# Performance work log

Measured on AMD Instinct MI355X. Metric: run time of the kernel, lower is better.

The kernel has to match this reference:

```python
import jax, jax.numpy as jnp
import numpy as np

LOG_SIG_MIN, LOG_SIG_MAX = -20.0, 2.0
BN_EPS = 1e-5

def leaky_relu(x):
    return jnp.where(x >= 0, x, 0.01 * x)

def setup_inputs() -> dict:
    key = jax.random.key(0)
    ks = jax.random.split(key, 12)
    E, B, N, H, A = 8, 16384, 64, 512, 8  # encoders, batch, nagents, hidden, heads
    d = H // A
    f32 = jnp.float32
    inp = {}
    inp['states'] = jax.random.normal(ks[0], (E, B, N), dtype=f32)
    inp['pre_actions'] = jax.random.normal(ks[1], (B, H), dtype=f32)
    inp['W_enc'] = jax.random.normal(ks[2], (E, N, H), dtype=f32) / np.sqrt(N)
    inp['b_enc'] = jnp.zeros((E, H), dtype=f32)
    inp['W_pre'] = jax.random.normal(ks[3], (H, H), dtype=f32) / np.sqrt(H)
    inp['b_pre'] = jnp.zeros((H,), dtype=f32)
    inp['Wk'] = jax.random.normal(ks[4], (A, H, d), dtype=f32) / np.sqrt(H)
    inp['Wsel'] = jax.random.normal(ks[5], (A, H, d), dtype=f32) / np.sqrt(H)
    inp['Wv'] = jax.random.normal(ks[6], (A, H, d), dtype=f32) / np.sqrt(H)
    inp['bv'] = jnp.zeros((A, d), dtype=f32)
    inp['W_actor'] = jax.random.normal(ks[7], (H, H), dtype=f32) / np.sqrt(H)
    inp['b_actor'] = jnp.zeros((H,), dtype=f32)
    inp['W_mean'] = jax.random.normal(ks[8], (H, N), dtype=f32) / np.sqrt(H)
    inp['b_mean'] = jnp.zeros((N,), dtype=f32)
    inp['W_logstd'] = jax.random.normal(ks[9], (H, N), dtype=f32) / np.sqrt(H)
    inp['b_logstd'] = jnp.zeros((N,), dtype=f32)
    return inp

def reference(states, pre_actions, W_enc, b_enc, W_pre, b_pre, Wk, Wsel, Wv, bv,
              W_actor, b_actor, W_mean, b_mean, W_logstd, b_logstd):
    # states: [E, B, N]; per-encoder BatchNorm1d (training-mode batch stats, no affine)
    mu = states.mean(axis=1, keepdims=True)                      # [E,1,N]
    var = states.var(axis=1, keepdims=True)                      # biased var, as torch BN
    s_norm = (states - mu) * jax.lax.rsqrt(var + BN_EPS)
    # per-encoder Linear + LeakyReLU -> encodings [E, B, H]
    encs = leaky_relu(jnp.einsum('ebn,enh->ebh', s_norm, W_enc) + b_enc[:, None, :])
    # per-head keys/values over all encoders: [A, E, B, d]
    keys = jnp.einsum('ebh,ahd->aebd', encs, Wk)
    vals = leaky_relu(jnp.einsum('ebh,ahd->aebd', encs, Wv) + bv[:, None, None, :])
    # selector from encoded previous actions: [A, B, d]
    pre = leaky_relu(pre_actions @ W_pre + b_pre)                 # [B, H]
    sel = jnp.einsum('bh,ahd->abd', pre, Wsel)
    d = keys.shape[-1]
    logits = jnp.einsum('abd,aebd->abe', sel, keys)               # [A, B, E]
    w = jax.nn.softmax(logits / np.sqrt(d), axis=-1)
    attn = jnp.einsum('aebd,abe->abd', vals, w)                   # [A, B, d]
    B = attn.shape[1]
    actor_in = jnp.transpose(attn, (1, 0, 2)).reshape(B, -1)      # [B, A*d] head-concat
    x = jax.nn.relu(actor_in @ W_actor + b_actor)
    mean = x @ W_mean + b_mean
    log_std = jnp.clip(x @ W_logstd + b_logstd, LOG_SIG_MIN, LOG_SIG_MAX)
    return mean, log_std, actor_in
```

## Files before the change

### kernel.cpp

```cpp
#include <hip/hip_runtime.h>
#include <hip/hip_bf16.h>
#include <stdint.h>

#define E_ 8
#define B_ 16384
#define N_ 64
#define H_ 512
#define A_ 8
#define D_ 64

typedef __hip_bfloat16 bf16;
typedef __attribute__((ext_vector_type(8))) short s8v;
typedef __attribute__((ext_vector_type(4))) float f4v;

__device__ __forceinline__ float bf2f(bf16 v) { return __bfloat162float(v); }
__device__ __forceinline__ bf16 f2bf(float v) { return __float2bfloat16(v); }
__device__ __forceinline__ short f2bfs(float v) {
    bf16 b = f2bf(v); short s; __builtin_memcpy(&s, &b, 2); return s;
}
__device__ __forceinline__ float bfs2f(short s) {
    bf16 b; __builtin_memcpy(&b, &s, 2); return bf2f(b);
}

__device__ __forceinline__ void async_load16(const void* g, void* l) {
    __builtin_amdgcn_global_load_lds(
        (const __attribute__((address_space(1))) void*)g,
        (__attribute__((address_space(3))) void*)l, 16, 0, 0);
}

__device__ __forceinline__ int swz_off(int row, int krow) {
    return row * 64 + (((krow >> 3) ^ (row & 7)) << 3);
}

__device__ __forceinline__ int swz32(int row, int g) {
    return row * 32 + ((g ^ ((row >> 1) & 3)) << 3);
}

template <int CB>
__device__ __forceinline__ void xcd_map(int x, int nBm, int& bm, int& bn) {
    if ((nBm & 7) == 0) {
        int j = x & 7, s = x >> 3;
        bn = s & ((1 << CB) - 1);
        bm = ((s >> CB) << 3) | j;
    } else {
        bm = x >> CB;
        bn = x & ((1 << CB) - 1);
    }
}

__global__ __launch_bounds__(256) void bnPart(const float* __restrict__ states,
                                              float* __restrict__ part,
                                              bf16* __restrict__ sbf) {
    int blk = blockIdx.x;
    int e = blk >> 6, sl = blk & 63;
    int tid = threadIdx.x, n = tid & 63, rg = tid >> 6;
    const long rowBase = (long)e * B_ + (long)sl * 256;
    const float* base = states + rowBase * 64;
    float s1 = 0.f, s2 = 0.f;
    for (int i = 0; i < 64; ++i) {
        float v = base[(rg + i * 4) * 64 + n];
        s1 += v; s2 += v * v;
        sbf[(rowBase + rg + i * 4) * 64 + n] = f2bf(v);
    }
    __shared__ float sh[2][4][64];
    sh[0][rg][n] = s1; sh[1][rg][n] = s2;
    __syncthreads();
    if (tid < 64) {
        float t1 = sh[0][0][n] + sh[0][1][n] + sh[0][2][n] + sh[0][3][n];
        float t2 = sh[1][0][n] + sh[1][1][n] + sh[1][2][n] + sh[1][3][n];
        part[((long)blk * 64 + n) * 2 + 0] = t1;
        part[((long)blk * 64 + n) * 2 + 1] = t2;
    }
}

__global__ void bnFin(const float* __restrict__ part, float* __restrict__ mu_rstd) {
    int idx = blockIdx.x * blockDim.x + threadIdx.x;
    if (idx >= E_ * 64) return;
    int e = idx >> 6, n = idx & 63;
    float s1 = 0.f, s2 = 0.f;
    for (int sl = 0; sl < 64; ++sl) {
        s1 += part[(((long)e * 64 + sl) * 64 + n) * 2 + 0];
        s2 += part[(((long)e * 64 + sl) * 64 + n) * 2 + 1];
    }
    float mu = s1 / (float)B_;
    float var = s2 / (float)B_ - mu * mu;
    mu_rstd[idx * 2 + 0] = mu;
    mu_rstd[idx * 2 + 1] = rsqrtf(var + 1e-5f);
}

__global__ void foldEnc(const float* __restrict__ W_enc, const float* __restrict__ b_enc,
                        const float* __restrict__ mu_rstd,
                        bf16* __restrict__ WencfT, float* __restrict__ bencf) {
    int idx = blockIdx.x * 256 + threadIdx.x;
    int e = idx >> 9, h = idx & 511;
    float acc = b_enc[e * 512 + h];
    for (int n = 0; n < 64; ++n) {
        float mu = mu_rstd[(e * 64 + n) * 2 + 0];
        float rs = mu_rstd[(e * 64 + n) * 2 + 1];
        float w = W_enc[((long)e * 64 + n) * 512 + h];
        WencfT[((long)e * 512 + h) * 64 + n] = f2bf(w * rs);
        acc -= mu * rs * w;
    }
    bencf[e * 512 + h] = acc;
}

__global__ __launch_bounds__(256) void packAll(
    const float* __restrict__ W_pre, const float* __restrict__ W_actor,
    const float* __restrict__ Wsel, const float* __restrict__ Wk,
    const float* __restrict__ Wv, const float* __restrict__ wm,
    const float* __restrict__ wl, const float* __restrict__ pre_actions,
    bf16* __restrict__ WpreT, bf16* __restrict__ WactorT, bf16* __restrict__ WselT,
    bf16* __restrict__ WkvaT, bf16* __restrict__ WmlT, bf16* __restrict__ pa_bf) {
    int bx = blockIdx.x, tid = threadIdx.x;
    if (bx < 2048) {
        const float* in = (bx < 1024) ? W_pre : W_actor;
        bf16* out = (bx < 1024) ? WpreT : WactorT;
        int idx = (bx & 1023) * 256 + tid;
        int n = idx >> 9, k = idx & 511;
        out[idx] = f2bf(in[k * 512 + n]);
    } else if (bx < 3072) {
        int idx = (bx - 2048) * 256 + tid;
        int n = idx >> 9, h = idx & 511;
        int a = n >> 6, dd = n & 63;
        WselT[idx] = f2bf(Wsel[((long)a * 512 + h) * 64 + dd]);
    } else if (bx < 5120) {
        int idx = (bx - 3072) * 256 + tid;
        int n = idx >> 9, h = idx & 511;
        int a = n >> 7, j = n & 127;
        const float* src = (j < 64) ? Wk : Wv;
        WkvaT[idx] = f2bf(src[((long)a * 512 + h) * 64 + (j & 63)]);
    } else if (bx < 5376) {
        int idx = (bx - 5120) * 256 + tid;
        int n = idx >> 9, k = idx & 511;
        float v = (n < 64) ? wm[k * 64 + n] : wl[k * 64 + (n - 64)];
        WmlT[idx] = f2bf(v);
    } else {
        int i = (bx - 5376) * 256 + tid;
        float4 v = ((const float4*)pre_actions)[i];
        bf16 o[4] = {f2bf(v.x), f2bf(v.y), f2bf(v.z), f2bf(v.w)};
        __builtin_memcpy(pa_bf + (long)i * 4, o, 8);
    }
}

template <int ACT, int OUTF, bool HAS_BIAS, int CB>
__global__ __launch_bounds__(256) void gemm_bt(
    const bf16* __restrict__ Ag, const bf16* __restrict__ Bg,
    const float* __restrict__ bias, const float* __restrict__ bias2,
    void* __restrict__ out, void* __restrict__ out2,
    int M, int Nn, int K, long sA, long sB, long sBias, long sO) {
    const int tid = threadIdx.x, lane = tid & 63, wid = tid >> 6;
    const int wm = wid >> 1, wn = wid & 1;
    int bm, bn;
    xcd_map<CB>(blockIdx.x, gridDim.x >> CB, bm, bn);
    const int bz = blockIdx.z;
    const bf16* Aptr = Ag + (long)bz * sA + (long)bm * 128 * K;
    const bf16* Bptr = Bg + (long)bz * sB + (long)bn * 128 * K;

    __shared__ __align__(16) short sAl[128 * 64];
    __shared__ __align__(16) short sBl[128 * 64];

    const int srow = lane >> 3;
    const int scol = (((lane & 7) ^ srow) << 3);

    f4v acc[4][4];
#pragma unroll
    for (int i = 0; i < 4; ++i)
#pragma unroll
        for (int j = 0; j < 4; ++j) acc[i][j] = f4v{0.f, 0.f, 0.f, 0.f};

    for (int k0 = 0; k0 < K; k0 += 64) {
#pragma unroll
        for (int i = 0; i < 4; ++i) {
            int r = (wid * 4 + i) * 8 + srow;
            async_load16(Aptr + (long)r * K + k0 + scol, (char*)sAl + (wid * 4 + i) * 1024);
            async_load16(Bptr + (long)r * K + k0 + scol, (char*)sBl + (wid * 4 + i) * 1024);
        }
        __syncthreads();
#pragma unroll
        for (int kk = 0; kk < 64; kk += 32) {
            int krow = kk + (lane >> 4) * 8;
            s8v af[4], bfr[4];
#pragma unroll
            for (int mi = 0; mi < 4; ++mi)
                af[mi] = *(const s8v*)(sAl + swz_off(wm * 64 + mi * 16 + (lane & 15), krow));
#pragma unroll
            for (int ni = 0; ni < 4; ++ni)
                bfr[ni] = *(const s8v*)(sBl + swz_off(wn * 64 + ni * 16 + (lane & 15), krow));
#pragma unroll
            for (int mi = 0; mi < 4; ++mi)
#pragma unroll
                for (int ni = 0; ni < 4; ++ni)
                    acc[mi][ni] = __builtin_amdgcn_mfma_f32_16x16x32_bf16(
                        af[mi], bfr[ni], acc[mi][ni], 0, 0, 0);
        }
        __syncthreads();
    }

    long m0 = (long)bm * 128 + wm * 64;
    long n0 = (long)bn * 128 + wn * 64;
#pragma unroll
    for (int mi = 0; mi < 4; ++mi)
#pragma unroll
        for (int ni = 0; ni < 4; ++ni)
#pragma unroll
            for (int r = 0; r < 4; ++r) {
                long gm = m0 + mi * 16 + (lane >> 4) * 4 + r;
                long gn = n0 + ni * 16 + (lane & 15);
                float v = acc[mi][ni][r];
                if constexpr (HAS_BIAS) v += bias[sBias * bz + gn];
                if constexpr (ACT == 1) v = (v >= 0.f) ? v : 0.01f * v;
                if constexpr (ACT == 2) v = fmaxf(v, 0.f);
                if constexpr (OUTF == 0) {
                    ((bf16*)out)[(long)bz * sO + gm * Nn + gn] = f2bf(v);
                } else if constexpr (OUTF == 1) {
                    ((float*)out)[(long)bz * sO + gm * Nn + gn] = v;
                } else if constexpr (OUTF == 2) {
                    if (gn < 64) {
                        ((float*)out)[gm * 64 + gn] = v + bias[gn];
                    } else {
                        float w = v + bias2[gn - 64];
                        w = fminf(fmaxf(w, -20.f), 2.f);
                        ((float*)out2)[gm * 64 + (gn - 64)] = w;
                    }
                } else {
                    ((bf16*)out)[(gm * E_ + bz) * 512 + gn] = f2bf(v);
                }
            }
}

__global__ __launch_bounds__(256, 4) void kv_attn(
    const bf16* __restrict__ Ag, const bf16* __restrict__ Bg,
    const float* __restrict__ bv, const float* __restrict__ sel,
    float* __restrict__ actor_f32, bf16* __restrict__ attn_bf, int b0) {
    const int tid = threadIdx.x, lane = tid & 63, wid = tid >> 6;
    const int wm = wid >> 1, wn = wid & 1;
    int bm, a;
    xcd_map<3>(blockIdx.x, gridDim.x >> 3, bm, a);
    const bf16* Aptr = Ag + (long)bm * 128 * 512;
    const bf16* Bptr = Bg + (long)a * 128 * 512;

    __shared__ __align__(16) short smem[17408];
    __shared__ float lgs[128];

    const long bgBase = (long)b0 + (long)bm * 16;

    auto stage = [&](int kt, int buf) {
#pragma unroll
        for (int i = 0; i < 2; ++i) {
            int c = tid + i * 256;
            int r = c >> 2;
            int g = (c & 3) ^ ((r >> 1) & 3);
            async_load16(Aptr + (long)r * 512 + kt * 32 + g * 8,
                         (char*)smem + buf * 8192 + c * 16);
            async_load16(Bptr + (long)r * 512 + kt * 32 + g * 8,
                         (char*)smem + 16384 + buf * 8192 + c * 16);
        }
    };

    f4v acc[4][4];
#pragma unroll
    for (int i = 0; i < 4; ++i)
#pragma unroll
        for (int j = 0; j < 4; ++j) acc[i][j] = f4v{0.f, 0.f, 0.f, 0.f};

    stage(0, 0);
    __syncthreads();
    int cur = 0;
    for (int t = 0; t < 16; ++t) {
        if (t < 15) stage(t + 1, cur ^ 1);
        const short* sAc = smem + cur * 4096;
        const short* sBc = smem + 8192 + cur * 4096;
        const int g = lane >> 4;
        s8v af[4], bfr[4];
#pragma unroll
        for (int mi = 0; mi < 4; ++mi)
            af[mi] = *(const s8v*)(sAc + swz32(wm * 64 + mi * 16 + (lane & 15), g));
#pragma unroll
        for (int ni = 0; ni < 4; ++ni)
            bfr[ni] = *(const s8v*)(sBc + swz32(wn * 64 + ni * 16 + (lane & 15), g));
#pragma unroll
        for (int mi = 0; mi < 4; ++mi)
#pragma unroll
            for (int ni = 0; ni < 4; ++ni)
                acc[mi][ni] = __builtin_amdgcn_mfma_f32_16x16x32_bf16(
                    af[mi], bfr[ni], acc[mi][ni], 0, 0, 0);
        __syncthreads();
        cur ^= 1;
    }

    short* keysC = smem;
    short* vT    = smem + 9216;
    const int quad = lane >> 4, cl = lane & 15;
#pragma unroll
    for (int mi = 0; mi < 4; ++mi)
#pragma unroll
        for (int ni = 0; ni < 4; ++ni)
#pragma unroll
            for (int r = 0; r < 4; ++r) {
                int row = wm * 64 + mi * 16 + quad * 4 + r;
                float v = acc[mi][ni][r];
                if (wn == 0) {
                    keysC[row * 72 + ni * 16 + cl] = f2bfs(v);
                } else {
                    int d = ni * 16 + cl;
                    v += bv[a * 64 + d];
                    v = (v >= 0.f) ? v : 0.01f * v;
                    vT[d * 128 + (row ^ ((d & 15) << 3))] = f2bfs(v);
                }
            }

    s8v bselH[2], bselL[2];
#pragma unroll
    for (int kk = 0; kk < 2; ++kk) {
        const float* sp = sel + (bgBase + cl) * 512 + a * 64 + kk * 32 + quad * 8;
#pragma unroll
        for (int j = 0; j < 8; ++j) {
            float s = sp[j] * 0.125f;
            short h = f2bfs(s);
            bselH[kk][j] = h;
            bselL[kk][j] = f2bfs(s - bfs2f(h));
        }
    }
    __syncthreads();

    {
        f4v lgacc[2] = {f4v{0.f, 0.f, 0.f, 0.f}, f4v{0.f, 0.f, 0.f, 0.f}};
#pragma unroll
        for (int kk = 0; kk < 2; ++kk) {
#pragma unroll
            for (int mi = 0; mi < 2; ++mi) {
                s8v af = *(const s8v*)(keysC + (wid * 32 + mi * 16 + cl) * 72 +
                                       kk * 32 + quad * 8);
                lgacc[mi] = __builtin_amdgcn_mfma_f32_16x16x32_bf16(
                    af, bselH[kk], lgacc[mi], 0, 0, 0);
                lgacc[mi] = __builtin_amdgcn_mfma_f32_16x16x32_bf16(
                    af, bselL[kk], lgacc[mi], 0, 0, 0);
            }
        }
#pragma unroll
        for (int mi = 0; mi < 2; ++mi)
#pragma unroll
            for (int r = 0; r < 4; ++r) {
                int grow = wid * 32 + mi * 16 + quad * 4 + r;
                if (cl == (grow >> 3)) lgs[grow] = lgacc[mi][r];
            }
    }
    __syncthreads();

#pragma unroll
    for (int t = 0; t < 4; ++t) {
        int lb = wid * 4 + t, row0 = lb * 8;
        s8v vvv = *(const s8v*)(vT + lane * 128 + (row0 ^ ((lane & 15) << 3)));
        float lg[8], vv[8];
#pragma unroll
        for (int e = 0; e < 8; ++e) {
            vv[e] = bfs2f(vvv[e]);
            lg[e] = lgs[row0 + e];
        }
        float mx = lg[0];
#pragma unroll
        for (int e = 1; e < 8; ++e) mx = fmaxf(mx, lg[e]);
        float ssum = 0.f, w[8];
#pragma unroll
        for (int e = 0; e < 8; ++e) { w[e] = __expf(lg[e] - mx); ssum += w[e]; }
        float inv = 1.f / ssum;
        float at = 0.f;
#pragma unroll
        for (int e = 0; e < 8; ++e) at += vv[e] * (w[e] * inv);
        long o = (bgBase + lb) * 512 + a * 64 + lane;
        actor_f32[o] = at;
        attn_bf[o] = f2bf(at);
    }
}

extern "C" void kernel_launch(void* const* d_in, const int* in_sizes, int n_in,
                              void* d_out, int out_size, void* d_ws, size_t ws_size,
                              hipStream_t stream) {
    (void)in_sizes; (void)n_in; (void)out_size;
    const float* states      = (const float*)d_in[0];
    const float* pre_actions = (const float*)d_in[1];
    const float* W_enc       = (const float*)d_in[2];
    const float* b_enc       = (const float*)d_in[3];
    const float* W_pre       = (const float*)d_in[4];
    const float* b_pre       = (const float*)d_in[5];
    const float* Wk          = (const float*)d_in[6];
    const float* Wsel        = (const float*)d_in[7];
    const float* Wv          = (const float*)d_in[8];
    const float* bv          = (const float*)d_in[9];
    const float* W_actor     = (const float*)d_in[10];
    const float* b_actor     = (const float*)d_in[11];
    const float* W_mean      = (const float*)d_in[12];
    const float* b_mean      = (const float*)d_in[13];
    const float* W_logstd    = (const float*)d_in[14];
    const float* b_logstd    = (const float*)d_in[15];

    char* ws = (char*)d_ws;
    size_t off = 0;
    auto alloc = [&](size_t bytes) -> void* {
        void* p = ws + off;
        off = (off + bytes + 255) & ~(size_t)255;
        return p;
    };
    float* mu_rstd = (float*)alloc((size_t)E_ * 64 * 2 * 4);
    float* bnpart  = (float*)alloc((size_t)E_ * 64 * 64 * 2 * 4);
    bf16* WencfT   = (bf16*)alloc((size_t)E_ * 512 * 64 * 2);
    float* bencf   = (float*)alloc((size_t)E_ * 512 * 4);
    bf16* WpreT    = (bf16*)alloc((size_t)512 * 512 * 2);
    bf16* WselT    = (bf16*)alloc((size_t)512 * 512 * 2);
    bf16* WkvaT    = (bf16*)alloc((size_t)1024 * 512 * 2);
    bf16* WactorT  = (bf16*)alloc((size_t)512 * 512 * 2);
    bf16* WmlT     = (bf16*)alloc((size_t)128 * 512 * 2);
    bf16* pa_bf    = (bf16*)alloc((size_t)B_ * 512 * 2);
    bf16* p_pre    = (bf16*)alloc((size_t)B_ * 512 * 2);
    float* p_sel   = (float*)alloc((size_t)B_ * 512 * 4);
    bf16* s_bf     = (bf16*)alloc((size_t)E_ * B_ * 64 * 2);
    bf16* p_attn = pa_bf;
    bf16* p_x    = p_pre;

    size_t remaining = (ws_size > off) ? ws_size - off : 0;
    int Bc = B_;
    while (Bc > 128 && (size_t)Bc * 8192 + 4096 > remaining) Bc >>= 1;
    const int NC = B_ / Bc;
    bf16* c_encs = (bf16*)alloc((size_t)E_ * Bc * 512 * 2);

    packAll<<<13568, 256, 0, stream>>>(W_pre, W_actor, Wsel, Wk, Wv, W_mean, W_logstd,
                                       pre_actions, WpreT, WactorT, WselT, WkvaT, WmlT,
                                       pa_bf);
    bnPart<<<512, 256, 0, stream>>>(states, bnpart, s_bf);
    bnFin<<<2, 256, 0, stream>>>(bnpart, mu_rstd);
    foldEnc<<<16, 256, 0, stream>>>(W_enc, b_enc, mu_rstd, WencfT, bencf);

    gemm_bt<1, 0, true, 2><<<dim3((B_ / 128) << 2, 1, 1), 256, 0, stream>>>(
        pa_bf, WpreT, b_pre, nullptr, p_pre, nullptr, B_, 512, 512, 0, 0, 0, 0);
    gemm_bt<0, 1, false, 2><<<dim3((B_ / 128) << 2, 1, 1), 256, 0, stream>>>(
        p_pre, WselT, nullptr, nullptr, p_sel, nullptr, B_, 512, 512, 0, 0, 0, 0);

    float* actor_out = (float*)d_out + 2L * B_ * 64;
    for (int c = 0; c < NC; ++c) {
        int b0 = c * Bc;
        gemm_bt<1, 4, true, 2><<<dim3((Bc / 128) << 2, 1, E_), 256, 0, stream>>>(
            s_bf + (long)b0 * 64, WencfT, bencf, nullptr, c_encs, nullptr, Bc, 512, 64,
            (long)B_ * 64, (long)512 * 64, 512, 0);
        kv_attn<<<dim3((Bc / 16) * 8, 1, 1), 256, 0, stream>>>(
            c_encs, WkvaT, bv, p_sel, actor_out, p_attn, b0);
    }

    gemm_bt<2, 0, true, 2><<<dim3((B_ / 128) << 2, 1, 1), 256, 0, stream>>>(
        p_attn, WactorT, b_actor, nullptr, p_x, nullptr, B_, 512, 512, 0, 0, 0, 0);
    gemm_bt<0, 2, false, 0><<<dim3(B_ / 128, 1, 1), 256, 0, stream>>>(
        p_x, WmlT, b_mean, b_logstd, (float*)d_out, (float*)d_out + (long)B_ * 64,
        B_, 128, 512, 0, 0, 0, 0);
}
```

Measured before the change: 482.8 us.

## Double-buffer GEMM K-loop with 64x128 tiles and higher occupancy

Rewrites the shared GEMM kernel to use 64-row M tiles with K steps of 32, and double-buffers shared memory so the async global-to-LDS load of the next K tile overlaps the MFMA work on the current one. This removes one barrier per iteration and the load stall. Launch bounds now request 4 blocks per SM, and grids are doubled to match the smaller tiles. In exchange each tile reuses data less, so global traffic for the B operand rises, and register pressure is capped.

```diff
diff --git a/kernel.cpp b/kernel.cpp
--- a/kernel.cpp
+++ b/kernel.cpp
@@ -26,10 +26,6 @@
     __builtin_amdgcn_global_load_lds(
         (const __attribute__((address_space(1))) void*)g,
         (__attribute__((address_space(3))) void*)l, 16, 0, 0);
-}
-
-__device__ __forceinline__ int swz_off(int row, int krow) {
-    return row * 64 + (((krow >> 3) ^ (row & 7)) << 3);
 }
 
 __device__ __forceinline__ int swz32(int row, int g) {
@@ -143,7 +139,7 @@
 }
 
 template <int ACT, int OUTF, bool HAS_BIAS, int CB>
-__global__ __launch_bounds__(256) void gemm_bt(
+__global__ __launch_bounds__(256, 4) void gemm_bt2(
     const bf16* __restrict__ Ag, const bf16* __restrict__ Bg,
     const float* __restrict__ bias, const float* __restrict__ bias2,
     void* __restrict__ out, void* __restrict__ out2,
@@ -153,59 +149,70 @@
     int bm, bn;
     xcd_map<CB>(blockIdx.x, gridDim.x >> CB, bm, bn);
     const int bz = blockIdx.z;
-    const bf16* Aptr = Ag + (long)bz * sA + (long)bm * 128 * K;
+    const bf16* Aptr = Ag + (long)bz * sA + (long)bm * 64 * K;
     const bf16* Bptr = Bg + (long)bz * sB + (long)bn * 128 * K;
 
-    __shared__ __align__(16) short sAl[128 * 64];
-    __shared__ __align__(16) short sBl[128 * 64];
-
-    const int srow = lane >> 3;
-    const int scol = (((lane & 7) ^ srow) << 3);
-
-    f4v acc[4][4];
-#pragma unroll
-    for (int i = 0; i < 4; ++i)
+    __shared__ __align__(16) short smem[12288];
+
+    auto stage = [&](int kt, int buf) {
+        {
+            int c = tid, r = c >> 2;
+            int g = (c & 3) ^ ((r >> 1) & 3);
+            async_load16(Aptr + (long)r * K + kt * 32 + g * 8,
+                         (char*)smem + buf * 4096 + c * 16);
+        }
+#pragma unroll
+        for (int i = 0; i < 2; ++i) {
+            int c = tid + i * 256, r = c >> 2;
+            int g = (c & 3) ^ ((r >> 1) & 3);
+            async_load16(Bptr + (long)r * K + kt * 32 + g * 8,
+                         (char*)smem + 8192 + buf * 8192 + c * 16);
+        }
+    };
+
+    f4v acc[2][4];
+#pragma unroll
+    for (int i = 0; i < 2; ++i)
 #pragma unroll
         for (int j = 0; j < 4; ++j) acc[i][j] = f4v{0.f, 0.f, 0.f, 0.f};
 
-    for (int k0 = 0; k0 < K; k0 += 64) {
-#pragma unroll
-        for (int i = 0; i < 4; ++i) {
-            int r = (wid * 4 + i) * 8 + srow;
-            async_load16(Aptr + (long)r * K + k0 + scol, (char*)sAl + (wid * 4 + i) * 1024);
-            async_load16(Bptr + (long)r * K + k0 + scol, (char*)sBl + (wid * 4 + i) * 1024);
-        }
+    stage(0, 0);
+    __syncthreads();
+    int cur = 0;
+    const int nt = K >> 5;
+    for (int t = 0; t < nt; ++t) {
+        if (t < nt - 1) stage(t + 1, cur ^ 1);
+        const short* sAc = smem + cur * 2048;
+        const short* sBc = smem + 4096 + cur * 4096;
+        const int g = lane >> 4;
+        s8v af[2], bfr[4];
+#pragma unroll
+        for (int mi = 0; mi < 2; ++mi)
+            af[mi] = *(const s8v*)(sAc + swz32(wm * 32 + mi * 16 + (lane & 15), g));
+#pragma unroll
+        for (int ni = 0; ni < 4; ++ni)
+            bfr[ni] = *(const s8v*)(sBc + swz32(wn * 64 + ni * 16 + (lane & 15), g));
+#pragma unroll
+        for (int mi = 0; mi < 2; ++mi)
+#pragma unroll
+            for (int ni = 0; ni < 4; ++ni)
+                acc[mi][ni] = __builtin_amdgcn_mfma_f32_16x16x32_bf16(
+                    af[mi], bfr[ni], acc[mi][ni], 0, 0, 0);
         __syncthreads();
-#pragma unroll
-        for (int kk = 0; kk < 64; kk += 32) {
-            int krow = kk + (lane >> 4) * 8;
-            s8v af[4], bfr[4];
-#pragma unroll
-            for (int mi = 0; mi < 4; ++mi)
-                af[mi] = *(const s8v*)(sAl + swz_off(wm * 64 + mi * 16 + (lane & 15), krow));
-#pragma unroll
-            for (int ni = 0; ni < 4; ++ni)
-                bfr[ni] = *(const s8v*)(sBl + swz_off(wn * 64 + ni * 16 + (lane & 15), krow));
-#pragma unroll
-            for (int mi = 0; mi < 4; ++mi)
-#pragma unroll
-                for (int ni = 0; ni < 4; ++ni)
-                    acc[mi][ni] = __builtin_amdgcn_mfma_f32_16x16x32_bf16(
-                        af[mi], bfr[ni], acc[mi][ni], 0, 0, 0);
-        }
-        __syncthreads();
-    }
-
-    long m0 = (long)bm * 128 + wm * 64;
+        cur ^= 1;
+    }
+
+    long m0 = (long)bm * 64 + wm * 32;
     long n0 = (long)bn * 128 + wn * 64;
-#pragma unroll
-    for (int mi = 0; mi < 4; ++mi)
+    const int quad = lane >> 4, cl = lane & 15;
+#pragma unroll
+    for (int mi = 0; mi < 2; ++mi)
 #pragma unroll
         for (int ni = 0; ni < 4; ++ni)
 #pragma unroll
             for (int r = 0; r < 4; ++r) {
-                long gm = m0 + mi * 16 + (lane >> 4) * 4 + r;
-                long gn = n0 + ni * 16 + (lane & 15);
+                long gm = m0 + mi * 16 + quad * 4 + r;
+                long gn = n0 + ni * 16 + cl;
                 float v = acc[mi][ni][r];
                 if constexpr (HAS_BIAS) v += bias[sBias * bz + gn];
                 if constexpr (ACT == 1) v = (v >= 0.f) ? v : 0.01f * v;
@@ -430,24 +437,24 @@
     bnFin<<<2, 256, 0, stream>>>(bnpart, mu_rstd);
     foldEnc<<<16, 256, 0, stream>>>(W_enc, b_enc, mu_rstd, WencfT, bencf);
 
-    gemm_bt<1, 0, true, 2><<<dim3((B_ / 128) << 2, 1, 1), 256, 0, stream>>>(
+    gemm_bt2<1, 0, true, 2><<<dim3((B_ / 64) << 2, 1, 1), 256, 0, stream>>>(
         pa_bf, WpreT, b_pre, nullptr, p_pre, nullptr, B_, 512, 512, 0, 0, 0, 0);
-    gemm_bt<0, 1, false, 2><<<dim3((B_ / 128) << 2, 1, 1), 256, 0, stream>>>(
+    gemm_bt2<0, 1, false, 2><<<dim3((B_ / 64) << 2, 1, 1), 256, 0, stream>>>(
         p_pre, WselT, nullptr, nullptr, p_sel, nullptr, B_, 512, 512, 0, 0, 0, 0);
 
     float* actor_out = (float*)d_out + 2L * B_ * 64;
     for (int c = 0; c < NC; ++c) {
         int b0 = c * Bc;
-        gemm_bt<1, 4, true, 2><<<dim3((Bc / 128) << 2, 1, E_), 256, 0, stream>>>(
+        gemm_bt2<1, 4, true, 2><<<dim3((Bc / 64) << 2, 1, E_), 256, 0, stream>>>(
             s_bf + (long)b0 * 64, WencfT, bencf, nullptr, c_encs, nullptr, Bc, 512, 64,
             (long)B_ * 64, (long)512 * 64, 512, 0);
         kv_attn<<<dim3((Bc / 16) * 8, 1, 1), 256, 0, stream>>>(
             c_encs, WkvaT, bv, p_sel, actor_out, p_attn, b0);
     }
 
-    gemm_bt<2, 0, true, 2><<<dim3((B_ / 128) << 2, 1, 1), 256, 0, stream>>>(
+    gemm_bt2<2, 0, true, 2><<<dim3((B_ / 64) << 2, 1, 1), 256, 0, stream>>>(
         p_attn, WactorT, b_actor, nullptr, p_x, nullptr, B_, 512, 512, 0, 0, 0, 0);
-    gemm_bt<0, 2, false, 0><<<dim3(B_ / 128, 1, 1), 256, 0, stream>>>(
+    gemm_bt2<0, 2, false, 0><<<dim3(B_ / 64, 1, 1), 256, 0, stream>>>(
         p_x, WmlT, b_mean, b_logstd, (float*)d_out, (float*)d_out + (long)B_ * 64,
         B_, 128, 512, 0, 0, 0, 0);
 }
```

Result: faster. 460.9 us (-4.5%).
